# Performance work log

Hardware: AMD Instinct MI355X
Metric: run time of the kernel (lower is better)

Reference implementation:

```python
import jax, jax.numpy as jnp
import numpy as np

N = 200000   # nodes in graph / memory bank
E = 300000   # edges with features
B = 300      # interactions in batch
K = 10       # temporal neighbors per hop
D = 172      # node feat dim = edge feat dim = time dim = memory dim
MSG = 100    # message dimension (message_function='mlp')
H = 2        # attention heads
QD = 2 * D   # query dim  (node emb + time enc)
KD = 3 * D   # key dim    (neigh emb + edge feat + time enc)
RAW = 4 * D + 1  # raw message dim: 2*mem + edge + time + num


def setup_inputs() -> dict:
    key = jax.random.key(0)
    ks = iter(jax.random.split(key, 48))
    def nrm(shape, s=0.05):
        return jax.random.normal(next(ks), shape, dtype=jnp.float32) * s
    def unif(shape, lo=0.0, hi=1.0):
        return jax.random.uniform(next(ks), shape, jnp.float32, lo, hi)
    zeros = lambda shape: jnp.zeros(shape, jnp.float32)
    # unique node ids so the scatter memory write is deterministic ('last' aggregator)
    perm = jax.random.permutation(next(ks), N).astype(jnp.int32)
    inp = {
        'node_features': nrm((N, D), 1.0),
        'edge_features': nrm((E, D), 1.0),
        'memory': nrm((N, D), 1.0),
        'last_update': unif((N,), 0.0, 1e4),
        'time_w': nrm((D,), 1.0),
        'time_b': nrm((D,), 1.0),
        'num_w1': nrm((1, 1)), 'num_b1': zeros((1,)),
        'num_w2': nrm((1, 1)), 'num_b2': zeros((1,)),
        'msg_w1': nrm((RAW, RAW // 2)), 'msg_b1': zeros((RAW // 2,)),
        'msg_w2': nrm((RAW // 2, MSG)), 'msg_b2': zeros((MSG,)),
        'gru_wih': nrm((3 * D, MSG)), 'gru_whh': nrm((3 * D, D)),
        'gru_bih': zeros((3 * D,)), 'gru_bhh': zeros((3 * D,)),
        'att_wq': nrm((2, QD, QD)), 'att_wk': nrm((2, KD, QD)), 'att_wv': nrm((2, KD, QD)),
        'att_bq': zeros((2, QD)), 'att_bk': zeros((2, QD)), 'att_bv': zeros((2, QD)),
        'att_wo': nrm((2, QD, QD)), 'att_bo': zeros((2, QD)),
        'mrg_w1': nrm((2, QD + D, D)), 'mrg_b1': zeros((2, D)),
        'mrg_w2': nrm((2, D, D)), 'mrg_b2': zeros((2, D)),
        'edge_times': unif((B,), 0.0, 1e4),
        'num_conn': unif((B,), 0.0, 20.0),
        'n1_et': unif((3 * B, K), 0.0, 1e4),
        'n2_et': unif((3 * B * K, K), 0.0, 1e4),
        'src': perm[:B], 'dst': perm[B:2 * B], 'neg': perm[2 * B:3 * B],
        'edge_idxs': jax.random.randint(next(ks), (B,), 0, E, jnp.int32),
        'n1_nb': jax.random.randint(next(ks), (3 * B, K), 0, N, jnp.int32),
        'n1_eidx': jax.random.randint(next(ks), (3 * B, K), 0, E, jnp.int32),
        'n2_nb': jax.random.randint(next(ks), (3 * B * K, K), 0, N, jnp.int32),
        'n2_eidx': jax.random.randint(next(ks), (3 * B * K, K), 0, E, jnp.int32),
    }
    return inp


def reference(node_features, edge_features, memory, last_update, time_w, time_b,
              num_w1, num_b1, num_w2, num_b2,
              msg_w1, msg_b1, msg_w2, msg_b2,
              gru_wih, gru_whh, gru_bih, gru_bhh,
              att_wq, att_wk, att_wv, att_bq, att_bk, att_bv, att_wo, att_bo,
              mrg_w1, mrg_b1, mrg_w2, mrg_b2,
              edge_times, num_conn, n1_et, n2_et,
              src, dst, neg, edge_idxs, n1_nb, n1_eidx, n2_nb, n2_eidx):
    def time_enc(t):  # TimeEncode: cos(t * w + b)
        return jnp.cos(t[..., None] * time_w + time_b)

    def gru(x, h):  # torch.nn.GRUCell math
        gi = x @ gru_wih.T + gru_bih
        gh = h @ gru_whh.T + gru_bhh
        ir, iz, i_n = jnp.split(gi, 3, axis=-1)
        hr, hz, h_n = jnp.split(gh, 3, axis=-1)
        r = jax.nn.sigmoid(ir + hr)
        z = jax.nn.sigmoid(iz + hz)
        n = jnp.tanh(i_n + r * h_n)
        return (1.0 - z) * n + z * h

    # ---- message computation + GRU memory update (memory_update_at_start) ----
    num_e = jax.nn.relu(num_conn[:, None] @ num_w1 + num_b1) @ num_w2 + num_b2  # [B,1]
    ef = edge_features[edge_idxs]                                               # [B,D]
    def make_msg(a, b):
        raw = jnp.concatenate(
            [memory[a], memory[b], ef, time_enc(edge_times - last_update[a]), num_e], -1)
        return jax.nn.relu(raw @ msg_w1 + msg_b1) @ msg_w2 + msg_b2
    mem = memory.at[src].set(gru(make_msg(src, dst), memory[src]))
    mem = mem.at[dst].set(gru(make_msg(dst, src), memory[dst]))

    def feat(n):  # layer-0 features: memory + raw node features
        return mem[n] + node_features[n]

    def attention(l, src_conv, ts, nb, neigh_emb, efeat, et):
        # src_conv [n,D]; neigh_emb [n,K,D]; efeat [n,K,D]; et [n,K]
        q_in = jnp.concatenate([src_conv, time_enc(jnp.zeros_like(ts))], -1)        # [n,QD]
        k_in = jnp.concatenate([neigh_emb, efeat, time_enc(ts[:, None] - et)], -1)  # [n,K,KD]
        q = q_in @ att_wq[l] + att_bq[l]
        k = k_in @ att_wk[l] + att_bk[l]
        v = k_in @ att_wv[l] + att_bv[l]
        n, Kn = nb.shape
        dh = q.shape[-1] // H
        qh = q.reshape(n, H, dh)
        kh = k.reshape(n, Kn, H, dh)
        vh = v.reshape(n, Kn, H, dh)
        scores = jnp.einsum('nhd,nkhd->nhk', qh, kh) / jnp.sqrt(jnp.float32(dh))
        mask = (nb == 0)  # padded neighbors
        scores = jnp.where(mask[:, None, :], -1e9, scores)
        attn = jax.nn.softmax(scores, axis=-1)
        out = jnp.einsum('nhk,nkhd->nhd', attn, vh).reshape(n, H * dh)
        out = out @ att_wo[l] + att_bo[l]
        out = jnp.where(jnp.all(mask, axis=-1)[:, None], 0.0, out)  # invalid neighborhoods
        # MergeLayer(query_dim, D, D, D)
        h = jax.nn.relu(jnp.concatenate([out, src_conv], -1) @ mrg_w1[l] + mrg_b1[l])
        return h @ mrg_w2[l] + mrg_b2[l]

    nodes = jnp.concatenate([src, dst, neg])   # [3B]
    ts = jnp.tile(edge_times, 3)               # [3B]
    Kn = n1_nb.shape[1]
    # layer-1 embedding of target nodes (attention model 0)
    src_conv = attention(0, feat(nodes), ts, n1_nb, feat(n1_nb), edge_features[n1_eidx], n1_et)
    # layer-1 embedding of first-hop neighbors, at repeated interaction times
    n1_flat = n1_nb.reshape(-1)
    ts_rep = jnp.repeat(ts, Kn)
    neigh1 = attention(0, feat(n1_flat), ts_rep, n2_nb, feat(n2_nb),
                       edge_features[n2_eidx], n2_et)
    # layer-2 aggregation (attention model 1)
    emb = attention(1, src_conv, ts, n1_nb,
                    neigh1.reshape(nodes.shape[0], Kn, -1), edge_features[n1_eidx], n1_et)
    return emb  # [3B, D]: src / dst / neg temporal embeddings
```

## Files before the change

### kernel.cpp

```cpp
#include <hip/hip_runtime.h>
#include <math.h>

#define NN 200000
#define BB 300
#define KK 10
#define DD 172
#define R0T 9900
#define R0P 9984
#define L1P 1024
#define QIN_K 384
#define KIN_K 576
#define H_K 192
#define CK 1088
#define QKN 1034
#define QKLD 1040
#define GROWS 1152

typedef short bfrag __attribute__((ext_vector_type(8)));
typedef float f4 __attribute__((ext_vector_type(4)));

__device__ inline unsigned short f2b(float f) {
  unsigned int u = __builtin_bit_cast(unsigned int, f);
  u += 0x7fffu + ((u >> 16) & 1u);
  return (unsigned short)(u >> 16);
}
__device__ inline float b2f(unsigned short s) {
  unsigned int u = ((unsigned int)s) << 16;
  return __builtin_bit_cast(float, u);
}
__device__ inline float sigm(float x) { return 1.f / (1.f + expf(-x)); }

__global__ __launch_bounds__(256) void fill_map(int* map) {
  int i = blockIdx.x * 256 + threadIdx.x;
  if (i < NN) map[i] = -1;
}
__global__ __launch_bounds__(64) void set_map(int* map, const int* src, const int* dst) {
  int i = blockIdx.x * 64 + threadIdx.x;
  if (i < BB) { map[src[i]] = i; map[dst[i]] = BB + i; }
}

#define SZ_WQH (2*2*384*192)
#define SZ_WKH (2*2*640*192)
#define SZ_WVH (2*2*640*192)
#define SZ_WOT (2*2*384*192)
#define SZ_M1  (2*256*576)
#define SZ_M2  (2*256*192)
#define SZ_MW1 (384*704)
#define SZ_MW2 (128*384)
#define SZ_GIH (640*128)
#define SZ_GHH (640*192)
__global__ __launch_bounds__(256) void prep_w(
    const float* wq, const float* wk, const float* wv, const float* wo,
    const float* m1, const float* m2, const float* mw1, const float* mw2,
    const float* gih, const float* ghh,
    unsigned short* wqh_b, unsigned short* wkh_b, unsigned short* wvh_b,
    unsigned short* woT_b, unsigned short* wm1_t, unsigned short* wm2_t,
    unsigned short* msgw1t, unsigned short* msgw2t,
    unsigned short* gruwih_b, unsigned short* gruwhh_b) {
  long idx = (long)blockIdx.x * 256 + threadIdx.x;
  if (idx < SZ_WQH) {
    int l = idx / (2*384*192), r = idx % (2*384*192);
    int h = r / (384*192); r %= 384*192;
    int y = r / 192, d = r % 192;
    wqh_b[idx] = (y < 344 && d < 172) ? f2b(wq[(size_t)l*344*344 + (size_t)y*344 + h*172 + d]) : 0;
    return;
  }
  idx -= SZ_WQH;
  if (idx < SZ_WKH) {
    int l = idx / (2*640*192), r = idx % (2*640*192);
    int h = r / (640*192); r %= 640*192;
    int x = r / 192, d = r % 192;
    wkh_b[idx] = (x < 516 && d < 172) ? f2b(wk[(size_t)l*516*344 + (size_t)x*344 + h*172 + d]) : 0;
    return;
  }
  idx -= SZ_WKH;
  if (idx < SZ_WVH) {
    int l = idx / (2*640*192), r = idx % (2*640*192);
    int h = r / (640*192); r %= 640*192;
    int x = r / 192, d = r % 192;
    wvh_b[idx] = (x < 516 && d < 172) ? f2b(wv[(size_t)l*516*344 + (size_t)x*344 + h*172 + d]) : 0;
    return;
  }
  idx -= SZ_WVH;
  if (idx < SZ_WOT) {
    int l = idx / (2*384*192), r = idx % (2*384*192);
    int h = r / (384*192); r %= 384*192;
    int j = r / 192, d = r % 192;
    woT_b[idx] = (j < 344 && d < 172) ? f2b(wo[(size_t)l*344*344 + (size_t)(h*172+d)*344 + j]) : 0;
    return;
  }
  idx -= SZ_WOT;
  if (idx < SZ_M1) {
    int l = idx / (256*576), r = idx % (256*576);
    int j = r / 576, k = r % 576;
    wm1_t[idx] = (j < 172 && k < 516) ? f2b(m1[(size_t)l*516*172 + (size_t)k*172 + j]) : 0;
    return;
  }
  idx -= SZ_M1;
  if (idx < SZ_M2) {
    int l = idx / (256*192), r = idx % (256*192);
    int j = r / 192, k = r % 192;
    wm2_t[idx] = (j < 172 && k < 172) ? f2b(m2[(size_t)l*172*172 + (size_t)k*172 + j]) : 0;
    return;
  }
  idx -= SZ_M2;
  if (idx < SZ_MW1) {
    int j = idx / 704, k = idx % 704;
    msgw1t[idx] = (j < 344 && k < 689) ? f2b(mw1[(size_t)k*344 + j]) : 0;
    return;
  }
  idx -= SZ_MW1;
  if (idx < SZ_MW2) {
    int j = idx / 384, k = idx % 384;
    msgw2t[idx] = (j < 100 && k < 344) ? f2b(mw2[(size_t)k*100 + j]) : 0;
    return;
  }
  idx -= SZ_MW2;
  if (idx < SZ_GIH) {
    int j = idx / 128, k = idx % 128;
    gruwih_b[idx] = (j < 516 && k < 100) ? f2b(gih[(size_t)j*100 + k]) : 0;
    return;
  }
  idx -= SZ_GIH;
  if (idx < SZ_GHH) {
    int j = idx / 192, k = idx % 192;
    gruwhh_b[idx] = (j < 516 && k < 172) ? f2b(ghh[(size_t)j*172 + k]) : 0;
    return;
  }
}

#define SB_QK (2*QKLD)
#define SB_VO (2*344)
#define SB_GV (2*2*384)
__global__ __launch_bounds__(256) void prep_bias(
    const float* wq, const float* wk, const float* wo,
    const float* bq, const float* bk, const float* bv, const float* bo,
    float* bqk, float* bvwo, unsigned short* Gcat) {
  long idx = (long)blockIdx.x * 256 + threadIdx.x;
  if (idx < SB_QK) {
    int l = idx / QKLD, x = idx % QKLD;
    float acc = 0.f;
    if (x < 1032) {
      int h = x / 516, xx = x % 516;
      for (int d = 0; d < 172; d++)
        acc += wk[(size_t)l*516*344 + (size_t)xx*344 + h*172 + d] * bq[(size_t)l*344 + h*172 + d];
    } else if (x < 1034) {
      int h = x - 1032;
      for (int d = 0; d < 172; d++)
        acc += bq[(size_t)l*344 + h*172 + d] * bk[(size_t)l*344 + h*172 + d];
    }
    bqk[idx] = acc;
    return;
  }
  idx -= SB_QK;
  if (idx < SB_VO) {
    int l = idx / 344, j = idx % 344;
    float acc = bo[(size_t)l*344 + j];
    for (int c = 0; c < 344; c++)
      acc += bv[(size_t)l*344 + c] * wo[(size_t)l*344*344 + (size_t)c*344 + j];
    bvwo[idx] = acc;
    return;
  }
  idx -= SB_VO;
  if (idx < SB_GV) {
    int l = idx / (2*384), r = idx % (2*384);
    int h = r / 384, y = r % 384;
    float acc = 0.f;
    if (y < 344)
      for (int d = 0; d < 172; d++)
        acc += wq[(size_t)l*344*344 + (size_t)y*344 + h*172 + d] * bk[(size_t)l*344 + h*172 + d];
    Gcat[(size_t)l*GROWS*384 + (size_t)(1032+h)*384 + y] = (y < 344) ? f2b(acc) : 0;
    return;
  }
}

template<bool OBF, bool RELU>
__global__ __launch_bounds__(256) void gemm128(
    const unsigned short* __restrict__ A, int lda,
    const unsigned short* __restrict__ Bt, int ldb,
    const float* __restrict__ bias,
    void* __restrict__ Cv, int ldc, int M, int N, int Nz, int Kpad) {
  __shared__ __align__(16) unsigned short As[128][72];
  __shared__ __align__(16) unsigned short Bs[128][72];
  const int tid = threadIdx.x;
  const int lane = tid & 63, w = tid >> 6;
  const int rbase = (w >> 1) * 64, cbase = (w & 1) * 64;
  const int fr = lane & 15, fq = lane >> 4;
  const size_t Arow0 = (size_t)blockIdx.x * 128;
  const size_t Brow0 = (size_t)blockIdx.y * 128;
  f4 acc[4][4];
#pragma unroll
  for (int a = 0; a < 4; a++)
#pragma unroll
    for (int b = 0; b < 4; b++)
#pragma unroll
      for (int r = 0; r < 4; r++) acc[a][b][r] = 0.f;

  const int srow = tid >> 3, sch = tid & 7;
  for (int k0 = 0; k0 < Kpad; k0 += 64) {
#pragma unroll
    for (int p = 0; p < 4; p++) {
      int row = srow + p * 32;
      *(uint4*)&As[row][sch * 8] = *(const uint4*)(A + (Arow0 + row) * lda + k0 + sch * 8);
      *(uint4*)&Bs[row][sch * 8] = *(const uint4*)(Bt + (Brow0 + row) * ldb + k0 + sch * 8);
    }
    __syncthreads();
#pragma unroll
    for (int s = 0; s < 2; s++) {
      bfrag a[4], b[4];
#pragma unroll
      for (int mt = 0; mt < 4; mt++) a[mt] = *(const bfrag*)&As[rbase + mt*16 + fr][s*32 + fq*8];
#pragma unroll
      for (int nt = 0; nt < 4; nt++) b[nt] = *(const bfrag*)&Bs[cbase + nt*16 + fr][s*32 + fq*8];
#pragma unroll
      for (int mt = 0; mt < 4; mt++)
#pragma unroll
        for (int nt = 0; nt < 4; nt++)
          acc[mt][nt] = __builtin_amdgcn_mfma_f32_16x16x32_bf16(a[mt], b[nt], acc[mt][nt], 0, 0, 0);
    }
    __syncthreads();
  }
#pragma unroll
  for (int mt = 0; mt < 4; mt++) {
#pragma unroll
    for (int nt = 0; nt < 4; nt++) {
      int gc = (int)Brow0 + cbase + nt * 16 + fr;
      float bias_v = (bias != nullptr && gc < N) ? bias[gc] : 0.f;
#pragma unroll
      for (int r = 0; r < 4; r++) {
        int gr = (int)Arow0 + rbase + mt * 16 + fq * 4 + r;
        if (gr < M && gc < Nz) {
          float v = 0.f;
          if (gc < N) {
            v = acc[mt][nt][r] + bias_v;
            if (RELU) v = fmaxf(v, 0.f);
          }
          if (OBF) ((unsigned short*)Cv)[(size_t)gr * ldc + gc] = f2b(v);
          else     ((float*)Cv)[(size_t)gr * ldc + gc] = v;
        }
      }
    }
  }
}

__global__ __launch_bounds__(256) void build_raw(
    const float* memory, const float* edge_features, const float* last_update,
    const float* time_w, const float* time_b,
    const float* num_w1, const float* num_b1, const float* num_w2, const float* num_b2,
    const float* edge_times, const float* num_conn,
    const int* src, const int* dst, const int* edge_idxs,
    unsigned short* raw, unsigned short* memb) {
  const int r = blockIdx.x, t = threadIdx.x;
  const int e = (r < BB) ? r : r - BB;
  const int a = (r < BB) ? src[e] : dst[e];
  const int b = (r < BB) ? dst[e] : src[e];
  const int ei = edge_idxs[e];
  const float dt = edge_times[e] - last_update[a];
  for (int c = t; c < 704; c += 256) {
    float v;
    if (c < 172) v = memory[(size_t)a*DD + c];
    else if (c < 344) v = memory[(size_t)b*DD + (c-172)];
    else if (c < 516) v = edge_features[(size_t)ei*DD + (c-344)];
    else if (c < 688) { int d = c-516; v = cosf(dt * time_w[d] + time_b[d]); }
    else if (c == 688) v = fmaxf(num_conn[e]*num_w1[0]+num_b1[0], 0.f)*num_w2[0]+num_b2[0];
    else v = 0.f;
    raw[(size_t)r*704 + c] = f2b(v);
  }
  for (int d = t; d < 192; d += 256)
    memb[(size_t)r*192 + d] = (d < 172) ? f2b(memory[(size_t)a*DD + d]) : 0;
}

__global__ __launch_bounds__(192) void gru_gate(
    const float* gi, const float* gh, const float* memory,
    const int* src, const int* dst, float* upd) {
  int r = blockIdx.x, t = threadIdx.x;
  int a = (r < BB) ? src[r] : dst[r - BB];
  if (t < DD) {
    float i_r = gi[(size_t)r*516 + t], i_z = gi[(size_t)r*516 + DD + t], i_n = gi[(size_t)r*516 + 2*DD + t];
    float h_r = gh[(size_t)r*516 + t], h_z = gh[(size_t)r*516 + DD + t], h_n = gh[(size_t)r*516 + 2*DD + t];
    float rr = sigm(i_r + h_r);
    float z  = sigm(i_z + h_z);
    float nn = tanhf(i_n + rr * h_n);
    float h  = memory[(size_t)a*DD + t];
    upd[(size_t)r*DD + t] = (1.f - z) * nn + z * h;
  }
}

__global__ __launch_bounds__(256) void build_qin0(
    const int* src, const int* dst, const int* neg, const int* n1_nb,
    const float* memory, const float* upd, const int* map, const float* nf,
    const float* time_b, unsigned short* qin) {
  int i = blockIdx.x, t = threadIdx.x;
  int node = (i < BB) ? src[i] : (i < 2*BB) ? dst[i-BB] : (i < 3*BB) ? neg[i-2*BB] : n1_nb[i-3*BB];
  int m = map[node];
  const float* mrow = (m >= 0) ? upd + (size_t)m*DD : memory + (size_t)node*DD;
  for (int c = t; c < QIN_K; c += 256) {
    unsigned short v;
    if (c < DD) v = f2b(mrow[c] + nf[(size_t)node*DD + c]);
    else if (c < 2*DD) v = f2b(cosf(time_b[c - DD]));
    else v = 0;
    qin[(size_t)i*QIN_K + c] = v;
  }
}

__global__ __launch_bounds__(256) void build_qin1(
    const unsigned short* conv0, const float* time_b, unsigned short* qin1) {
  int i = blockIdx.x, t = threadIdx.x;
  for (int c = t; c < QIN_K; c += 256) {
    unsigned short v;
    if (c < DD) v = conv0[(size_t)i*DD + c];
    else if (c < 2*DD) v = f2b(cosf(time_b[c - DD]));
    else v = 0;
    qin1[(size_t)i*QIN_K + c] = v;
  }
}

template <int MODE>
__global__ __launch_bounds__(256) void attn_core(
    const unsigned short* __restrict__ qk,
    const int* n1_nb, const int* n1_ei, const float* n1_et,
    const int* n2_nb, const int* n2_ei, const float* n2_et,
    const float* edge_times,
    const float* memory, const float* upd, const int* map, const float* nf,
    const unsigned short* conv0,
    const float* ef, const float* time_w, const float* time_b,
    unsigned short* __restrict__ C) {
  __shared__ unsigned short s_kin[KK][520];
  __shared__ float s_qk[1032];
  __shared__ float s_part[20][8];
  __shared__ float s_att[2][KK];
  __shared__ float s_qbk[2];
  __shared__ int s_nb[KK]; __shared__ int s_ei[KK]; __shared__ float s_et[KK];
  const int i = blockIdx.x, t = threadIdx.x;
  float ts;
  if (MODE == 0) {
    if (i < 3*BB) {
      if (t < KK) { s_nb[t] = n1_nb[(size_t)i*KK+t]; s_ei[t] = n1_ei[(size_t)i*KK+t]; s_et[t] = n1_et[(size_t)i*KK+t]; }
      ts = edge_times[i % BB];
    } else {
      int j = i - 3*BB;
      if (t < KK) { s_nb[t] = n2_nb[(size_t)j*KK+t]; s_ei[t] = n2_ei[(size_t)j*KK+t]; s_et[t] = n2_et[(size_t)j*KK+t]; }
      ts = edge_times[(j / KK) % BB];
    }
  } else {
    if (t < KK) { s_nb[t] = n1_nb[(size_t)i*KK+t]; s_ei[t] = n1_ei[(size_t)i*KK+t]; s_et[t] = n1_et[(size_t)i*KK+t]; }
    ts = edge_times[i % BB];
  }
  for (int c = t; c < 1032; c += 256) s_qk[c] = b2f(qk[(size_t)i*QKLD + c]);
  if (t < 2) s_qbk[t] = b2f(qk[(size_t)i*QKLD + 1032 + t]);
  __syncthreads();

  for (int f = t; f < KK*520; f += 256) {
    int k = f / 520, c = f - k * 520;
    unsigned short v;
    if (c < DD) {
      if (MODE == 0) {
        int nb = s_nb[k]; int m = map[nb];
        float x = ((m >= 0) ? upd[(size_t)m*DD + c] : memory[(size_t)nb*DD + c]) + nf[(size_t)nb*DD + c];
        v = f2b(x);
      } else {
        v = conv0[(size_t)(3*BB + i*KK + k)*DD + c];
      }
    } else if (c < 2*DD) {
      v = f2b(ef[(size_t)s_ei[k]*DD + (c - DD)]);
    } else if (c < 3*DD) {
      int d = c - 2*DD;
      v = f2b(cosf((ts - s_et[k]) * time_w[d] + time_b[d]));
    } else v = 0;
    s_kin[k][c] = v;
  }
  __syncthreads();

  if (t < 160) {
    int p = t >> 3, sub = t & 7;
    int h = p / KK, kk = p - h * KK;
    float acc = 0.f;
    for (int x = sub; x < 516; x += 8) acc += s_qk[h*516 + x] * b2f(s_kin[kk][x]);
    s_part[p][sub] = acc;
  }
  __syncthreads();
  if (t < 20) {
    float sc = 0.f;
    for (int s = 0; s < 8; s++) sc += s_part[t][s];
    int h = t / KK, kk = t - h * KK;
    sc = (sc + s_qbk[h]) * 0.07624928516630234f;
    if (s_nb[kk] == 0) sc = -1e9f;
    s_part[t][0] = sc;
  }
  __syncthreads();
  if (t < 2) {
    float mx = -1e30f;
    for (int kk = 0; kk < KK; kk++) mx = fmaxf(mx, s_part[t*KK + kk][0]);
    float e[KK], sum = 0.f;
    for (int kk = 0; kk < KK; kk++) { e[kk] = expf(s_part[t*KK + kk][0] - mx); sum += e[kk]; }
    float inv = 1.f / sum;
    for (int kk = 0; kk < KK; kk++) s_att[t][kk] = e[kk] * inv;
  }
  __syncthreads();

  for (int j = t; j < CK; j += 256) {
    float acc = 0.f;
    if (j < 1032) {
      int h = j / 516, x = j - h * 516;
#pragma unroll
      for (int kk = 0; kk < KK; kk++) acc += s_att[h][kk] * b2f(s_kin[kk][x]);
    }
    C[(size_t)i*CK + j] = f2b(acc);
  }
}

__global__ __launch_bounds__(256) void build_mrgA(
    const unsigned short* o2 , const int* nbA, const int* nbB, int split,
    const unsigned short* srcf, int ld_src, unsigned short* mrgA) {
  int i = blockIdx.x, t = threadIdx.x;
  const int* nbp = (i < split) ? nbA + (size_t)i*KK : nbB + (size_t)(i - split)*KK;
  __shared__ int allm;
  if (t == 0) {
    int a = 1;
    for (int k = 0; k < KK; k++) if (nbp[k] != 0) a = 0;
    allm = a;
  }
  __syncthreads();
  for (int c = t; c < KIN_K; c += 256) {
    unsigned short v;
    if (c < 2*DD) v = allm ? (unsigned short)0 : o2[(size_t)i*QIN_K + c];
    else if (c < 3*DD) v = srcf[(size_t)i*ld_src + (c - 2*DD)];
    else v = 0;
    mrgA[(size_t)i*KIN_K + c] = v;
  }
}

extern "C" void kernel_launch(void* const* d_in, const int* in_sizes, int n_in,
                              void* d_out, int out_size, void* d_ws, size_t ws_size,
                              hipStream_t stream) {
  const float* node_features = (const float*)d_in[0];
  const float* edge_features = (const float*)d_in[1];
  const float* memory        = (const float*)d_in[2];
  const float* last_update   = (const float*)d_in[3];
  const float* time_w        = (const float*)d_in[4];
  const float* time_b        = (const float*)d_in[5];
  const float* num_w1 = (const float*)d_in[6];
  const float* num_b1 = (const float*)d_in[7];
  const float* num_w2 = (const float*)d_in[8];
  const float* num_b2 = (const float*)d_in[9];
  const float* msg_w1 = (const float*)d_in[10];
  const float* msg_b1 = (const float*)d_in[11];
  const float* msg_w2 = (const float*)d_in[12];
  const float* msg_b2 = (const float*)d_in[13];
  const float* gru_wih = (const float*)d_in[14];
  const float* gru_whh = (const float*)d_in[15];
  const float* gru_bih = (const float*)d_in[16];
  const float* gru_bhh = (const float*)d_in[17];
  const float* att_wq = (const float*)d_in[18];
  const float* att_wk = (const float*)d_in[19];
  const float* att_wv = (const float*)d_in[20];
  const float* att_bq = (const float*)d_in[21];
  const float* att_bk = (const float*)d_in[22];
  const float* att_bv = (const float*)d_in[23];
  const float* att_wo = (const float*)d_in[24];
  const float* att_bo = (const float*)d_in[25];
  const float* mrg_w1 = (const float*)d_in[26];
  const float* mrg_b1 = (const float*)d_in[27];
  const float* mrg_w2 = (const float*)d_in[28];
  const float* mrg_b2 = (const float*)d_in[29];
  const float* edge_times = (const float*)d_in[30];
  const float* num_conn   = (const float*)d_in[31];
  const float* n1_et = (const float*)d_in[32];
  const float* n2_et = (const float*)d_in[33];
  const int* src = (const int*)d_in[34];
  const int* dst = (const int*)d_in[35];
  const int* neg = (const int*)d_in[36];
  const int* edge_idxs = (const int*)d_in[37];
  const int* n1_nb   = (const int*)d_in[38];
  const int* n1_eidx = (const int*)d_in[39];
  const int* n2_nb   = (const int*)d_in[40];
  const int* n2_eidx = (const int*)d_in[41];

  char* ws = (char*)d_ws;
  size_t off = 0;
  auto alloc = [&](size_t b) -> char* {
    char* p = ws + off; off = (off + b + 255) & ~(size_t)255; return p;
  };
  int* map  = (int*)alloc((size_t)NN * 4);
  float* upd = (float*)alloc((size_t)2*BB*DD * 4);
  unsigned short* wqh_b = (unsigned short*)alloc((size_t)SZ_WQH * 2);
  unsigned short* wkh_b = (unsigned short*)alloc((size_t)SZ_WKH * 2);
  unsigned short* wvh_b = (unsigned short*)alloc((size_t)SZ_WVH * 2);
  unsigned short* woT_b = (unsigned short*)alloc((size_t)SZ_WOT * 2);
  unsigned short* wm1_t = (unsigned short*)alloc((size_t)SZ_M1 * 2);
  unsigned short* wm2_t = (unsigned short*)alloc((size_t)SZ_M2 * 2);
  unsigned short* msgw1t = (unsigned short*)alloc((size_t)SZ_MW1 * 2);
  unsigned short* msgw2t = (unsigned short*)alloc((size_t)SZ_MW2 * 2);
  unsigned short* gruwih_b = (unsigned short*)alloc((size_t)SZ_GIH * 2);
  unsigned short* gruwhh_b = (unsigned short*)alloc((size_t)SZ_GHH * 2);
  unsigned short* Gcat = (unsigned short*)alloc((size_t)2*GROWS*384 * 2);
  unsigned short* Mcat = (unsigned short*)alloc((size_t)2*384*CK * 2);
  float* bqk  = (float*)alloc((size_t)2*QKLD * 4);
  float* bvwo = (float*)alloc((size_t)2*344 * 4);
  unsigned short* qin0 = (unsigned short*)alloc((size_t)R0P*QIN_K * 2);
  unsigned short* Cbuf = (unsigned short*)alloc((size_t)R0P*CK * 2);
  unsigned short* conv0 = (unsigned short*)alloc((size_t)R0P*DD * 2);

  char* T = ws + off;
  size_t mo = 0;
  auto ma = [&](size_t b) -> char* { char* p = T + mo; mo = (mo + b + 255) & ~(size_t)255; return p; };
  unsigned short* raw  = (unsigned short*)ma((size_t)640*704 * 2);
  unsigned short* memb = (unsigned short*)ma((size_t)640*192 * 2);
  unsigned short* h1m  = (unsigned short*)ma((size_t)640*384 * 2);
  unsigned short* msgb = (unsigned short*)ma((size_t)640*128 * 2);
  float* gi = (float*)ma((size_t)600*516 * 4);
  float* gh = (float*)ma((size_t)600*516 * 4);
  unsigned short* qk0 = (unsigned short*)T;
  size_t oo = 0;
  auto oa = [&](size_t b) -> char* { char* p = T + oo; oo = (oo + b + 255) & ~(size_t)255; return p; };
  unsigned short* o2_0  = (unsigned short*)oa((size_t)R0P*QIN_K * 2);
  unsigned short* mrgA0 = (unsigned short*)oa((size_t)R0P*KIN_K * 2);
  unsigned short* h0    = (unsigned short*)oa((size_t)R0P*H_K * 2);
  size_t lo = 0;
  auto la = [&](size_t b) -> char* { char* p = T + lo; lo = (lo + b + 255) & ~(size_t)255; return p; };
  unsigned short* qin1  = (unsigned short*)la((size_t)L1P*QIN_K * 2);
  unsigned short* qk1   = (unsigned short*)la((size_t)L1P*QKLD * 2);
  unsigned short* o2_1  = (unsigned short*)la((size_t)L1P*QIN_K * 2);
  unsigned short* mrgA1 = (unsigned short*)la((size_t)L1P*KIN_K * 2);
  unsigned short* h1b   = (unsigned short*)la((size_t)L1P*H_K * 2);

  fill_map<<<(NN + 255)/256, 256, 0, stream>>>(map);
  set_map<<<(BB + 63)/64, 64, 0, stream>>>(map, src, dst);
  {
    long tot = (long)SZ_WQH + SZ_WKH + SZ_WVH + SZ_WOT + SZ_M1 + SZ_M2 + SZ_MW1 + SZ_MW2 + SZ_GIH + SZ_GHH;
    prep_w<<<(int)((tot + 255)/256), 256, 0, stream>>>(
        att_wq, att_wk, att_wv, att_wo, mrg_w1, mrg_w2, msg_w1, msg_w2, gru_wih, gru_whh,
        wqh_b, wkh_b, wvh_b, woT_b, wm1_t, wm2_t, msgw1t, msgw2t, gruwih_b, gruwhh_b);
    long tb = (long)SB_QK + SB_VO + SB_GV;
    prep_bias<<<(int)((tb + 255)/256), 256, 0, stream>>>(
        att_wq, att_wk, att_wo, att_bq, att_bk, att_bv, att_bo, bqk, bvwo, Gcat);
  }
  for (int l = 0; l < 2; l++)
    for (int h = 0; h < 2; h++)
      gemm128<true, false><<<dim3(5, 3), 256, 0, stream>>>(
          wkh_b + (size_t)(l*2+h)*640*192, 192,
          wqh_b + (size_t)(l*2+h)*384*192, 192, nullptr,
          Gcat + (size_t)l*GROWS*384 + (size_t)h*516*384, 384, 516, 344, 384, 192);
  for (int l = 0; l < 2; l++)
    for (int h = 0; h < 2; h++)
      gemm128<true, false><<<dim3(3, 5), 256, 0, stream>>>(
          woT_b + (size_t)(l*2+h)*384*192, 192,
          wvh_b + (size_t)(l*2+h)*640*192, 192, nullptr,
          Mcat + (size_t)l*384*CK + (size_t)h*516, CK, 344, 516, (h == 0 ? 516 : 572), 192);

  build_raw<<<2*BB, 256, 0, stream>>>(
      memory, edge_features, last_update, time_w, time_b,
      num_w1, num_b1, num_w2, num_b2, edge_times, num_conn,
      src, dst, edge_idxs, raw, memb);
  gemm128<true, true><<<dim3(5, 3), 256, 0, stream>>>(
      raw, 704, msgw1t, 704, msg_b1, h1m, 384, 600, 344, 384, 704);
  gemm128<true, false><<<dim3(5, 1), 256, 0, stream>>>(
      h1m, 384, msgw2t, 384, msg_b2, msgb, 128, 600, 100, 128, 384);
  gemm128<false, false><<<dim3(5, 5), 256, 0, stream>>>(
      msgb, 128, gruwih_b, 128, gru_bih, gi, 516, 600, 516, 516, 128);
  gemm128<false, false><<<dim3(5, 5), 256, 0, stream>>>(
      memb, 192, gruwhh_b, 192, gru_bhh, gh, 516, 600, 516, 516, 192);
  gru_gate<<<2*BB, 192, 0, stream>>>(gi, gh, memory, src, dst, upd);

  build_qin0<<<R0T, 256, 0, stream>>>(src, dst, neg, n1_nb, memory, upd, map,
                                      node_features, time_b, qin0);
  gemm128<true, false><<<dim3(R0P/128, 9), 256, 0, stream>>>(
      qin0, QIN_K, Gcat, 384, bqk, qk0, QKLD, R0T, QKN, QKN, QIN_K);
  attn_core<0><<<R0T, 256, 0, stream>>>(
      qk0, n1_nb, n1_eidx, n1_et, n2_nb, n2_eidx, n2_et, edge_times,
      memory, upd, map, node_features, conv0,
      edge_features, time_w, time_b, Cbuf);
  gemm128<true, false><<<dim3(R0P/128, 3), 256, 0, stream>>>(
      Cbuf, CK, Mcat, CK, bvwo, o2_0, QIN_K, R0T, 344, 344, CK);
  build_mrgA<<<R0T, 256, 0, stream>>>(o2_0, n1_nb, n2_nb, 3*BB, qin0, QIN_K, mrgA0);
  gemm128<true, true><<<dim3(R0P/128, 2), 256, 0, stream>>>(
      mrgA0, KIN_K, wm1_t, KIN_K, mrg_b1, h0, H_K, R0T, 172, 192, KIN_K);
  gemm128<true, false><<<dim3(R0P/128, 2), 256, 0, stream>>>(
      h0, H_K, wm2_t, H_K, mrg_b2, conv0, DD, R0T, 172, 172, H_K);

  build_qin1<<<3*BB, 256, 0, stream>>>(conv0, time_b, qin1);
  gemm128<true, false><<<dim3(L1P/128, 9), 256, 0, stream>>>(
      qin1, QIN_K, Gcat + (size_t)GROWS*384, 384, bqk + QKLD, qk1, QKLD, 3*BB, QKN, QKN, QIN_K);
  attn_core<1><<<3*BB, 256, 0, stream>>>(
      qk1, n1_nb, n1_eidx, n1_et, n1_nb, n1_eidx, n1_et, edge_times,
      memory, upd, map, node_features, conv0,
      edge_features, time_w, time_b, Cbuf);
  gemm128<true, false><<<dim3(L1P/128, 3), 256, 0, stream>>>(
      Cbuf, CK, Mcat + (size_t)384*CK, CK, bvwo + 344, o2_1, QIN_K, 3*BB, 344, 344, CK);
  build_mrgA<<<3*BB, 256, 0, stream>>>(o2_1, n1_nb, n1_nb, 3*BB, conv0, DD, mrgA1);
  gemm128<true, true><<<dim3(L1P/128, 2), 256, 0, stream>>>(
      mrgA1, KIN_K, wm1_t + (size_t)256*KIN_K, KIN_K, mrg_b1 + 172, h1b, H_K, 3*BB, 172, 192, KIN_K);
  gemm128<false, false><<<dim3(L1P/128, 2), 256, 0, stream>>>(
      h1b, H_K, wm2_t + (size_t)256*H_K, H_K, mrg_b2 + 172, (float*)d_out, DD, 3*BB, 172, 172, H_K);
}
```

Measured before the change: 1.044 ms.

## Vectorize gather kernels and use MFMA for attention scores in attn_core

```diff
diff --git a/kernel.cpp b/kernel.cpp
--- a/kernel.cpp
+++ b/kernel.cpp
@@ -15,9 +15,11 @@
 #define QKN 1034
 #define QKLD 1040
 #define GROWS 1152
+#define KINLD 552
 
 typedef short bfrag __attribute__((ext_vector_type(8)));
 typedef float f4 __attribute__((ext_vector_type(4)));
+typedef unsigned short us4 __attribute__((ext_vector_type(4)));
 
 __device__ inline unsigned short f2b(float f) {
   unsigned int u = __builtin_bit_cast(unsigned int, f);
@@ -132,10 +134,12 @@
 #define SB_QK (2*QKLD)
 #define SB_VO (2*344)
 #define SB_GV (2*2*384)
+#define SB_CT 176
 __global__ __launch_bounds__(256) void prep_bias(
     const float* wq, const float* wk, const float* wo,
     const float* bq, const float* bk, const float* bv, const float* bo,
-    float* bqk, float* bvwo, unsigned short* Gcat) {
+    const float* time_b,
+    float* bqk, float* bvwo, unsigned short* Gcat, unsigned short* costb) {
   long idx = (long)blockIdx.x * 256 + threadIdx.x;
   if (idx < SB_QK) {
     int l = idx / QKLD, x = idx % QKLD;
@@ -170,6 +174,11 @@
       for (int d = 0; d < 172; d++)
         acc += wq[(size_t)l*344*344 + (size_t)y*344 + h*172 + d] * bk[(size_t)l*344 + h*172 + d];
     Gcat[(size_t)l*GROWS*384 + (size_t)(1032+h)*384 + y] = (y < 344) ? f2b(acc) : 0;
+    return;
+  }
+  idx -= SB_GV;
+  if (idx < SB_CT) {
+    costb[idx] = (idx < 172) ? f2b(cosf(time_b[idx])) : 0;
     return;
   }
 }
@@ -286,32 +295,46 @@
   }
 }
 
-__global__ __launch_bounds__(256) void build_qin0(
+__global__ __launch_bounds__(128) void build_qin0(
     const int* src, const int* dst, const int* neg, const int* n1_nb,
     const float* memory, const float* upd, const int* map, const float* nf,
-    const float* time_b, unsigned short* qin) {
-  int i = blockIdx.x, t = threadIdx.x;
-  int node = (i < BB) ? src[i] : (i < 2*BB) ? dst[i-BB] : (i < 3*BB) ? neg[i-2*BB] : n1_nb[i-3*BB];
-  int m = map[node];
-  const float* mrow = (m >= 0) ? upd + (size_t)m*DD : memory + (size_t)node*DD;
-  for (int c = t; c < QIN_K; c += 256) {
-    unsigned short v;
-    if (c < DD) v = f2b(mrow[c] + nf[(size_t)node*DD + c]);
-    else if (c < 2*DD) v = f2b(cosf(time_b[c - DD]));
-    else v = 0;
-    qin[(size_t)i*QIN_K + c] = v;
-  }
-}
-
-__global__ __launch_bounds__(256) void build_qin1(
-    const unsigned short* conv0, const float* time_b, unsigned short* qin1) {
-  int i = blockIdx.x, t = threadIdx.x;
-  for (int c = t; c < QIN_K; c += 256) {
-    unsigned short v;
-    if (c < DD) v = conv0[(size_t)i*DD + c];
-    else if (c < 2*DD) v = f2b(cosf(time_b[c - DD]));
-    else v = 0;
-    qin1[(size_t)i*QIN_K + c] = v;
+    const unsigned short* costb, unsigned short* qin) {
+  const int i = blockIdx.x, t = threadIdx.x;
+  if (t >= 96) return;
+  const int node = (i < BB) ? src[i] : (i < 2*BB) ? dst[i-BB] : (i < 3*BB) ? neg[i-2*BB] : n1_nb[i-3*BB];
+  unsigned short* row = qin + (size_t)i * QIN_K;
+  if (t < 43) {
+    const int m = map[node];
+    const float* mrow = (m >= 0) ? upd + (size_t)m*DD : memory + (size_t)node*DD;
+    const int c = t * 4;
+    f4 a = *(const f4*)(mrow + c);
+    f4 b = *(const f4*)(nf + (size_t)node*DD + c);
+    us4 o;
+    o[0] = f2b(a[0]+b[0]); o[1] = f2b(a[1]+b[1]); o[2] = f2b(a[2]+b[2]); o[3] = f2b(a[3]+b[3]);
+    *(us4*)(row + c) = o;
+  } else if (t < 86) {
+    const int c = (t - 43) * 4;
+    *(us4*)(row + 172 + c) = *(const us4*)(costb + c);
+  } else {
+    us4 z = {0,0,0,0};
+    *(us4*)(row + 344 + (t - 86) * 4) = z;
+  }
+}
+
+__global__ __launch_bounds__(128) void build_qin1(
+    const unsigned short* conv0, const unsigned short* costb, unsigned short* qin1) {
+  const int i = blockIdx.x, t = threadIdx.x;
+  if (t >= 96) return;
+  unsigned short* row = qin1 + (size_t)i * QIN_K;
+  if (t < 43) {
+    const int c = t * 4;
+    *(us4*)(row + c) = *(const us4*)(conv0 + (size_t)i*DD + c);
+  } else if (t < 86) {
+    const int c = (t - 43) * 4;
+    *(us4*)(row + 172 + c) = *(const us4*)(costb + c);
+  } else {
+    us4 z = {0,0,0,0};
+    *(us4*)(row + 344 + (t - 86) * 4) = z;
   }
 }
 
@@ -322,97 +345,157 @@
     const int* n2_nb, const int* n2_ei, const float* n2_et,
     const float* edge_times,
     const float* memory, const float* upd, const int* map, const float* nf,
-    const unsigned short* conv0,
+    const unsigned short* featb, int featld,
     const float* ef, const float* time_w, const float* time_b,
     unsigned short* __restrict__ C) {
-  __shared__ unsigned short s_kin[KK][520];
-  __shared__ float s_qk[1032];
-  __shared__ float s_part[20][8];
-  __shared__ float s_att[2][KK];
+  __shared__ __align__(16) unsigned short s_kin[KK][KINLD];
+  __shared__ __align__(16) unsigned short s_qkb[2][544];
+  __shared__ float s_att[2][16];
   __shared__ float s_qbk[2];
-  __shared__ int s_nb[KK]; __shared__ int s_ei[KK]; __shared__ float s_et[KK];
+  __shared__ int s_nb[KK];
+  __shared__ float s_dt[KK];
+  __shared__ const float* s_fr[KK];
+  __shared__ const unsigned short* s_br[KK];
+  __shared__ const float* s_er[KK];
   const int i = blockIdx.x, t = threadIdx.x;
-  float ts;
-  if (MODE == 0) {
-    if (i < 3*BB) {
-      if (t < KK) { s_nb[t] = n1_nb[(size_t)i*KK+t]; s_ei[t] = n1_ei[(size_t)i*KK+t]; s_et[t] = n1_et[(size_t)i*KK+t]; }
+  const int lane = t & 63, w = t >> 6;
+  const bool usebr = (MODE == 1) || (i < 3*BB);
+
+  for (int u = t; u < 272; u += 256) {
+    int h = u / 136, s = u - h * 136;
+    us4 v = {0,0,0,0};
+    int x;
+    if (s < 129) { x = s * 4; v = *(const us4*)(qk + (size_t)i*QKLD + h*516 + x); }
+    else x = 516 + (s - 129) * 4;
+    *(us4*)&s_qkb[h][x] = v;
+  }
+  if (t < 2) s_qbk[t] = b2f(qk[(size_t)i*QKLD + 1032 + t]);
+  if (t < KK) {
+    int nb, ei; float et, ts;
+    if (MODE == 0 && i >= 3*BB) {
+      int j = i - 3*BB;
+      nb = n2_nb[(size_t)j*KK + t]; ei = n2_ei[(size_t)j*KK + t]; et = n2_et[(size_t)j*KK + t];
+      ts = edge_times[(j / KK) % BB];
+    } else {
+      nb = n1_nb[(size_t)i*KK + t]; ei = n1_ei[(size_t)i*KK + t]; et = n1_et[(size_t)i*KK + t];
       ts = edge_times[i % BB];
+    }
+    s_nb[t] = nb;
+    s_dt[t] = ts - et;
+    s_er[t] = ef + (size_t)ei * DD;
+    if (usebr) {
+      s_br[t] = featb + (size_t)(3*BB + i*KK + t) * featld;
     } else {
-      int j = i - 3*BB;
-      if (t < KK) { s_nb[t] = n2_nb[(size_t)j*KK+t]; s_ei[t] = n2_ei[(size_t)j*KK+t]; s_et[t] = n2_et[(size_t)j*KK+t]; }
-      ts = edge_times[(j / KK) % BB];
-    }
-  } else {
-    if (t < KK) { s_nb[t] = n1_nb[(size_t)i*KK+t]; s_ei[t] = n1_ei[(size_t)i*KK+t]; s_et[t] = n1_et[(size_t)i*KK+t]; }
-    ts = edge_times[i % BB];
-  }
-  for (int c = t; c < 1032; c += 256) s_qk[c] = b2f(qk[(size_t)i*QKLD + c]);
-  if (t < 2) s_qbk[t] = b2f(qk[(size_t)i*QKLD + 1032 + t]);
+      int m = map[nb];
+      s_fr[t] = (m >= 0) ? upd + (size_t)m * DD : memory + (size_t)nb * DD;
+    }
+  }
   __syncthreads();
 
-  for (int f = t; f < KK*520; f += 256) {
-    int k = f / 520, c = f - k * 520;
-    unsigned short v;
-    if (c < DD) {
-      if (MODE == 0) {
-        int nb = s_nb[k]; int m = map[nb];
-        float x = ((m >= 0) ? upd[(size_t)m*DD + c] : memory[(size_t)nb*DD + c]) + nf[(size_t)nb*DD + c];
-        v = f2b(x);
+  for (int u = t; u < 1360; u += 256) {
+    if (u < 430) {
+      int k = u / 43, c = (u - k * 43) * 4;
+      us4 o;
+      if (usebr) {
+        o = *(const us4*)(s_br[k] + c);
       } else {
-        v = conv0[(size_t)(3*BB + i*KK + k)*DD + c];
+        f4 a = *(const f4*)(s_fr[k] + c);
+        f4 b = *(const f4*)(nf + (size_t)s_nb[k] * DD + c);
+        o[0] = f2b(a[0]+b[0]); o[1] = f2b(a[1]+b[1]); o[2] = f2b(a[2]+b[2]); o[3] = f2b(a[3]+b[3]);
       }
-    } else if (c < 2*DD) {
-      v = f2b(ef[(size_t)s_ei[k]*DD + (c - DD)]);
-    } else if (c < 3*DD) {
-      int d = c - 2*DD;
-      v = f2b(cosf((ts - s_et[k]) * time_w[d] + time_b[d]));
-    } else v = 0;
-    s_kin[k][c] = v;
+      *(us4*)&s_kin[k][c] = o;
+    } else if (u < 860) {
+      int v = u - 430;
+      int k = v / 43, c = (v - k * 43) * 4;
+      f4 e = *(const f4*)(s_er[k] + c);
+      us4 o;
+      o[0] = f2b(e[0]); o[1] = f2b(e[1]); o[2] = f2b(e[2]); o[3] = f2b(e[3]);
+      *(us4*)&s_kin[k][172 + c] = o;
+    } else if (u < 1290) {
+      int v = u - 860;
+      int k = v / 43, c = (v - k * 43) * 4;
+      float dt = s_dt[k];
+      f4 wv = *(const f4*)(time_w + c);
+      f4 bv = *(const f4*)(time_b + c);
+      us4 o;
+      o[0] = f2b(cosf(dt*wv[0]+bv[0])); o[1] = f2b(cosf(dt*wv[1]+bv[1]));
+      o[2] = f2b(cosf(dt*wv[2]+bv[2])); o[3] = f2b(cosf(dt*wv[3]+bv[3]));
+      *(us4*)&s_kin[k][344 + c] = o;
+    } else {
+      int v = u - 1290;
+      int k = v / 7, c = (v - k * 7) * 4;
+      us4 z = {0,0,0,0};
+      *(us4*)&s_kin[k][516 + c] = z;
+    }
   }
   __syncthreads();
 
-  if (t < 160) {
-    int p = t >> 3, sub = t & 7;
-    int h = p / KK, kk = p - h * KK;
-    float acc = 0.f;
-    for (int x = sub; x < 516; x += 8) acc += s_qk[h*516 + x] * b2f(s_kin[kk][x]);
-    s_part[p][sub] = acc;
+  if (w == 0) {
+    const unsigned short* arow = s_qkb[lane & 1];
+    int bc = lane & 15; bc = (bc > 9) ? 9 : bc;
+    const unsigned short* brow = s_kin[bc];
+    const int q8 = (lane >> 4) * 8;
+    f4 acc = {0.f, 0.f, 0.f, 0.f};
+#pragma unroll
+    for (int k0 = 0; k0 < 544; k0 += 32) {
+      bfrag a = *(const bfrag*)(arow + k0 + q8);
+      bfrag b = *(const bfrag*)(brow + k0 + q8);
+      acc = __builtin_amdgcn_mfma_f32_16x16x32_bf16(a, b, acc, 0, 0, 0);
+    }
+    float sc0 = -1e30f, sc1 = -1e30f;
+    if (lane < KK) {
+      sc0 = (acc[0] + s_qbk[0]) * 0.07624928516630234f;
+      sc1 = (acc[1] + s_qbk[1]) * 0.07624928516630234f;
+      if (s_nb[lane] == 0) { sc0 = -1e9f; sc1 = -1e9f; }
+    }
+    float m0 = sc0, m1 = sc1;
+#pragma unroll
+    for (int d = 1; d < 16; d <<= 1) {
+      m0 = fmaxf(m0, __shfl_xor(m0, d, 16));
+      m1 = fmaxf(m1, __shfl_xor(m1, d, 16));
+    }
+    float e0 = (lane < KK) ? expf(sc0 - m0) : 0.f;
+    float e1 = (lane < KK) ? expf(sc1 - m1) : 0.f;
+    float u0 = e0, u1 = e1;
+#pragma unroll
+    for (int d = 1; d < 16; d <<= 1) {
+      u0 += __shfl_xor(u0, d, 16);
+      u1 += __shfl_xor(u1, d, 16);
+    }
+    if (lane < 16) { s_att[0][lane] = e0 / u0; s_att[1][lane] = e1 / u1; }
   }
   __syncthreads();
-  if (t < 20) {
-    float sc = 0.f;
-    for (int s = 0; s < 8; s++) sc += s_part[t][s];
-    int h = t / KK, kk = t - h * KK;
-    sc = (sc + s_qbk[h]) * 0.07624928516630234f;
-    if (s_nb[kk] == 0) sc = -1e9f;
-    s_part[t][0] = sc;
-  }
-  __syncthreads();
-  if (t < 2) {
-    float mx = -1e30f;
-    for (int kk = 0; kk < KK; kk++) mx = fmaxf(mx, s_part[t*KK + kk][0]);
-    float e[KK], sum = 0.f;
-    for (int kk = 0; kk < KK; kk++) { e[kk] = expf(s_part[t*KK + kk][0] - mx); sum += e[kk]; }
-    float inv = 1.f / sum;
-    for (int kk = 0; kk < KK; kk++) s_att[t][kk] = e[kk] * inv;
-  }
-  __syncthreads();
-
-  for (int j = t; j < CK; j += 256) {
-    float acc = 0.f;
-    if (j < 1032) {
-      int h = j / 516, x = j - h * 516;
-#pragma unroll
-      for (int kk = 0; kk < KK; kk++) acc += s_att[h][kk] * b2f(s_kin[kk][x]);
-    }
-    C[(size_t)i*CK + j] = f2b(acc);
-  }
-}
-
-__global__ __launch_bounds__(256) void build_mrgA(
+
+  unsigned short* Crow = C + (size_t)i * CK;
+  if (t < 129) {
+    const int x = t * 4;
+    f4 a0 = {0.f,0.f,0.f,0.f}, a1 = {0.f,0.f,0.f,0.f};
+#pragma unroll
+    for (int k = 0; k < KK; k++) {
+      us4 v = *(const us4*)&s_kin[k][x];
+      float w0 = s_att[0][k], w1 = s_att[1][k];
+#pragma unroll
+      for (int j = 0; j < 4; j++) {
+        float f = b2f(v[j]);
+        a0[j] += w0 * f;
+        a1[j] += w1 * f;
+      }
+    }
+    us4 o0, o1;
+#pragma unroll
+    for (int j = 0; j < 4; j++) { o0[j] = f2b(a0[j]); o1[j] = f2b(a1[j]); }
+    *(us4*)(Crow + x) = o0;
+    *(us4*)(Crow + 516 + x) = o1;
+  } else if (t < 143) {
+    us4 z = {0,0,0,0};
+    *(us4*)(Crow + 1032 + (t - 129) * 4) = z;
+  }
+}
+
+__global__ __launch_bounds__(192) void build_mrgA(
     const unsigned short* o2 , const int* nbA, const int* nbB, int split,
     const unsigned short* srcf, int ld_src, unsigned short* mrgA) {
-  int i = blockIdx.x, t = threadIdx.x;
+  const int i = blockIdx.x, t = threadIdx.x;
   const int* nbp = (i < split) ? nbA + (size_t)i*KK : nbB + (size_t)(i - split)*KK;
   __shared__ int allm;
   if (t == 0) {
@@ -421,12 +504,19 @@
     allm = a;
   }
   __syncthreads();
-  for (int c = t; c < KIN_K; c += 256) {
-    unsigned short v;
-    if (c < 2*DD) v = allm ? (unsigned short)0 : o2[(size_t)i*QIN_K + c];
-    else if (c < 3*DD) v = srcf[(size_t)i*ld_src + (c - 2*DD)];
-    else v = 0;
-    mrgA[(size_t)i*KIN_K + c] = v;
+  if (t >= 144) return;
+  unsigned short* row = mrgA + (size_t)i * KIN_K;
+  if (t < 86) {
+    const int c = t * 4;
+    us4 v = {0,0,0,0};
+    if (!allm) v = *(const us4*)(o2 + (size_t)i*QIN_K + c);
+    *(us4*)(row + c) = v;
+  } else if (t < 129) {
+    const int c = (t - 86) * 4;
+    *(us4*)(row + 344 + c) = *(const us4*)(srcf + (size_t)i*ld_src + c);
+  } else {
+    us4 z = {0,0,0,0};
+    *(us4*)(row + 516 + (t - 129) * 4) = z;
   }
 }
 
@@ -497,6 +587,7 @@
   unsigned short* Mcat = (unsigned short*)alloc((size_t)2*384*CK * 2);
   float* bqk  = (float*)alloc((size_t)2*QKLD * 4);
   float* bvwo = (float*)alloc((size_t)2*344 * 4);
+  unsigned short* costb = (unsigned short*)alloc((size_t)256 * 2);
   unsigned short* qin0 = (unsigned short*)alloc((size_t)R0P*QIN_K * 2);
   unsigned short* Cbuf = (unsigned short*)alloc((size_t)R0P*CK * 2);
   unsigned short* conv0 = (unsigned short*)alloc((size_t)R0P*DD * 2);
@@ -531,9 +622,9 @@
     prep_w<<<(int)((tot + 255)/256), 256, 0, stream>>>(
         att_wq, att_wk, att_wv, att_wo, mrg_w1, mrg_w2, msg_w1, msg_w2, gru_wih, gru_whh,
         wqh_b, wkh_b, wvh_b, woT_b, wm1_t, wm2_t, msgw1t, msgw2t, gruwih_b, gruwhh_b);
-    long tb = (long)SB_QK + SB_VO + SB_GV;
+    long tb = (long)SB_QK + SB_VO + SB_GV + SB_CT;
     prep_bias<<<(int)((tb + 255)/256), 256, 0, stream>>>(
-        att_wq, att_wk, att_wo, att_bq, att_bk, att_bv, att_bo, bqk, bvwo, Gcat);
+        att_wq, att_wk, att_wo, att_bq, att_bk, att_bv, att_bo, time_b, bqk, bvwo, Gcat, costb);
   }
   for (int l = 0; l < 2; l++)
     for (int h = 0; h < 2; h++)
@@ -562,32 +653,32 @@
       memb, 192, gruwhh_b, 192, gru_bhh, gh, 516, 600, 516, 516, 192);
   gru_gate<<<2*BB, 192, 0, stream>>>(gi, gh, memory, src, dst, upd);
 
-  build_qin0<<<R0T, 256, 0, stream>>>(src, dst, neg, n1_nb, memory, upd, map,
-                                      node_features, time_b, qin0);
+  build_qin0<<<R0T, 128, 0, stream>>>(src, dst, neg, n1_nb, memory, upd, map,
+                                      node_features, costb, qin0);
   gemm128<true, false><<<dim3(R0P/128, 9), 256, 0, stream>>>(
       qin0, QIN_K, Gcat, 384, bqk, qk0, QKLD, R0T, QKN, QKN, QIN_K);
   attn_core<0><<<R0T, 256, 0, stream>>>(
       qk0, n1_nb, n1_eidx, n1_et, n2_nb, n2_eidx, n2_et, edge_times,
-      memory, upd, map, node_features, conv0,
+      memory, upd, map, node_features, qin0, QIN_K,
       edge_features, time_w, time_b, Cbuf);
   gemm128<true, false><<<dim3(R0P/128, 3), 256, 0, stream>>>(
       Cbuf, CK, Mcat, CK, bvwo, o2_0, QIN_K, R0T, 344, 344, CK);
-  build_mrgA<<<R0T, 256, 0, stream>>>(o2_0, n1_nb, n2_nb, 3*BB, qin0, QIN_K, mrgA0);
+  build_mrgA<<<R0T, 192, 0, stream>>>(o2_0, n1_nb, n2_nb, 3*BB, qin0, QIN_K, mrgA0);
   gemm128<true, true><<<dim3(R0P/128, 2), 256, 0, stream>>>(
       mrgA0, KIN_K, wm1_t, KIN_K, mrg_b1, h0, H_K, R0T, 172, 192, KIN_K);
   gemm128<true, false><<<dim3(R0P/128, 2), 256, 0, stream>>>(
       h0, H_K, wm2_t, H_K, mrg_b2, conv0, DD, R0T, 172, 172, H_K);
 
-  build_qin1<<<3*BB, 256, 0, stream>>>(conv0, time_b, qin1);
+  build_qin1<<<3*BB, 128, 0, stream>>>(conv0, costb, qin1);
   gemm128<true, false><<<dim3(L1P/128, 9), 256, 0, stream>>>(
       qin1, QIN_K, Gcat + (size_t)GROWS*384, 384, bqk + QKLD, qk1, QKLD, 3*BB, QKN, QKN, QIN_K);
   attn_core<1><<<3*BB, 256, 0, stream>>>(
       qk1, n1_nb, n1_eidx, n1_et, n1_nb, n1_eidx, n1_et, edge_times,
-      memory, upd, map, node_features, conv0,
+      memory, upd, map, node_features, conv0, DD,
       edge_features, time_w, time_b, Cbuf);
   gemm128<true, false><<<dim3(L1P/128, 3), 256, 0, stream>>>(
       Cbuf, CK, Mcat + (size_t)384*CK, CK, bvwo + 344, o2_1, QIN_K, 3*BB, 344, 344, CK);
-  build_mrgA<<<3*BB, 256, 0, stream>>>(o2_1, n1_nb, n1_nb, 3*BB, conv0, DD, mrgA1);
+  build_mrgA<<<3*BB, 192, 0, stream>>>(o2_1, n1_nb, n1_nb, 3*BB, conv0, DD, mrgA1);
   gemm128<true, true><<<dim3(L1P/128, 2), 256, 0, stream>>>(
       mrgA1, KIN_K, wm1_t + (size_t)256*KIN_K, KIN_K, mrg_b1 + 172, h1b, H_K, 3*BB, 172, 192, KIN_K);
   gemm128<false, false><<<dim3(L1P/128, 2), 256, 0, stream>>>(
```

New measurement: 930.1 us. 1.12x faster.
